# Performance work log

Hardware: AMD Instinct MI355X
Metric: run time of the kernel (lower is better)

The kernel has to match this reference:

```python
import jax, jax.numpy as jnp
import numpy as np


def setup_inputs() -> dict:
    key = jax.random.key(0)
    k1, k2 = jax.random.split(key)
    B, N, C = 128, 200000, 100
    values = jax.random.normal(k1, (B, N), dtype=jnp.float32)
    labels = jax.random.randint(k2, (N,), 0, C, dtype=jnp.int64)
    return {"values": values, "labels": labels, "num_classes": C}


def reference(values, labels, num_classes):
    # Stratified (label-grouped) max pooling:
    # values: [B, N], labels: [N] in [0, num_classes)
    # output: [B, num_classes], out[b, c] = max over columns j with labels[j] == c
    # segment_max reduces over the leading axis, so operate on values.T [N, B].
    pooled = jax.ops.segment_max(
        values.T, labels, num_segments=num_classes, indices_are_sorted=False
    )  # [C, B]
    return pooled.T  # [B, C]
```

## Files before the change

### kernel.cpp

```cpp
#include <hip/hip_runtime.h>
#include <hip/hip_bf16.h>


#define TPBS 512
#define COLS 512
#define SB   16
#define ENC_NEG_INF 0x007FFFFFu

__device__ __forceinline__ unsigned enc(float f) {
    unsigned u = __float_as_uint(f);
    return (u & 0x80000000u) ? ~u : (u | 0x80000000u);
}
__device__ __forceinline__ float dec(unsigned u) {
    unsigned b = (u & 0x80000000u) ? (u & 0x7FFFFFFFu) : ~u;
    return __uint_as_float(b);
}

__global__ __launch_bounds__(TPBS) void strat_scat(
    const float* __restrict__ values, const int* __restrict__ labels,
    unsigned* __restrict__ part, int B, int N, int C, int S) {
    extern __shared__ unsigned acc[];

    const int tid  = threadIdx.x;
    const int t    = blockIdx.x;
    const int rg   = blockIdx.y;
    const int row0 = rg * 64;
    const int rmax = min(64, B - row0);
    const int CW   = C * 65;

    for (int i = tid; i < CW; i += TPBS) acc[i] = ENC_NEG_INF;
    __syncthreads();

    const int jc = t * COLS + tid;
    if (jc < N) {
        const unsigned lab = (unsigned)labels[jc];
        unsigned* a = acc + lab * 65;
        const float* col = values + (size_t)row0 * N + jc;

        if (rmax == 64) {
            float v[2][16];
#pragma unroll
            for (int r = 0; r < 16; ++r) v[0][r] = col[(size_t)r * N];
#pragma unroll
            for (int b = 0; b < 4; ++b) {
                const int cur = b & 1;
                if (b < 3) {
#pragma unroll
                    for (int r = 0; r < 16; ++r)
                        v[cur ^ 1][r] = col[(size_t)((b + 1) * 16 + r) * N];
                }
#pragma unroll
                for (int r = 0; r < 16; ++r)
                    atomicMax(&a[b * 16 + r], enc(v[cur][r]));
            }
        } else {
            for (int r = 0; r < rmax; ++r)
                atomicMax(&a[r], enc(col[(size_t)r * N]));
        }
    }
    __syncthreads();

    unsigned* dst = part + (size_t)(rg * S + t) * ((size_t)C * 64);
    for (int i = tid; i < C * 64; i += TPBS)
        dst[i] = acc[(i >> 6) * 65 + (i & 63)];
}

__global__ __launch_bounds__(256) void strat_redA(
    const unsigned* __restrict__ part, unsigned* __restrict__ mid,
    int PC, int S, int RG) {
    const int total = RG * PC * SB;
    const int i = blockIdx.x * 256 + threadIdx.x;
    if (i >= total) return;
    const int sb  = i / (RG * PC);
    const int rem = i - sb * (RG * PC);
    const int rg  = rem / PC;
    const int q   = rem - rg * PC;

    const int chunk = (S + SB - 1) / SB;
    const int s0 = sb * chunk;
    const int s1 = min(S, s0 + chunk);

    const unsigned* p = part + ((size_t)rg * S) * PC + q;
    unsigned m0 = ENC_NEG_INF, m1 = ENC_NEG_INF, m2 = ENC_NEG_INF, m3 = ENC_NEG_INF;
    int s = s0;
    for (; s + 4 <= s1; s += 4) {
        m0 = max(m0, p[(size_t)(s + 0) * PC]);
        m1 = max(m1, p[(size_t)(s + 1) * PC]);
        m2 = max(m2, p[(size_t)(s + 2) * PC]);
        m3 = max(m3, p[(size_t)(s + 3) * PC]);
    }
    for (; s < s1; ++s) m0 = max(m0, p[(size_t)s * PC]);
    mid[i] = max(max(m0, m1), max(m2, m3));
}

__global__ __launch_bounds__(256) void strat_redB(
    const unsigned* __restrict__ mid, float* __restrict__ out,
    int B, int C, int RG) {
    const int PC = C * 64;
    const int i = blockIdx.x * 256 + threadIdx.x;
    if (i >= RG * PC) return;
    unsigned m = ENC_NEG_INF;
#pragma unroll
    for (int sb = 0; sb < SB; ++sb) m = max(m, mid[(size_t)sb * RG * PC + i]);
    const int rg = i / PC;
    const int q  = i - rg * PC;
    const int c  = q >> 6;
    const int l  = q & 63;
    const int b  = rg * 64 + l;
    if (b < B) out[b * C + c] = dec(m);
}


#define TPB   256
#define ROWS  8
#define FCPAD 257

__global__ __launch_bounds__(TPB) void strat_init(unsigned* __restrict__ out_enc, int n) {
    int i = blockIdx.x * TPB + threadIdx.x;
    if (i < n) out_enc[i] = ENC_NEG_INF;
}

__global__ __launch_bounds__(TPB) void strat_main_atomic(
    const float* __restrict__ values, const int* __restrict__ labels,
    unsigned* __restrict__ out_enc, int B, int N, int C, int T) {
    __shared__ unsigned acc[ROWS * FCPAD];
    const int tid  = threadIdx.x;
    const int row0 = blockIdx.y * ROWS;
    const int rmax = min(ROWS, B - row0);

    for (int i = tid; i < ROWS * FCPAD; i += TPB) acc[i] = ENC_NEG_INF;
    __syncthreads();

    const int t = blockIdx.x;
#pragma unroll
    for (int e = 0; e < 4; ++e) {
        const int j = t * 1024 + tid * 4 + e;
        if (j < N) {
            const int c = labels[j];
            for (int r = 0; r < rmax; ++r)
                atomicMax(&acc[r * FCPAD + c],
                          enc(values[(size_t)(row0 + r) * N + j]));
        }
    }
    __syncthreads();
    for (int i = tid; i < rmax * C; i += TPB) {
        const int r = i / C, c = i - r * C;
        atomicMax(&out_enc[(size_t)(row0 + r) * C + c], acc[r * FCPAD + c]);
    }
}

__global__ __launch_bounds__(TPB) void strat_decode(unsigned* __restrict__ buf, int n) {
    int i = blockIdx.x * TPB + threadIdx.x;
    if (i < n) {
        float f = dec(buf[i]);
        ((float*)buf)[i] = f;
    }
}


extern "C" void kernel_launch(void* const* d_in, const int* in_sizes, int n_in,
                              void* d_out, int out_size, void* d_ws, size_t ws_size,
                              hipStream_t stream) {
    const float* values = (const float*)d_in[0];
    const int*   labels = (const int*)d_in[1];
    const int N  = in_sizes[1];
    const int B  = in_sizes[0] / N;
    const int C  = out_size / B;
    const int RG = (B + 63) / 64;
    const int PC = C * 64;
    const int S  = (N + COLS - 1) / COLS;

    const size_t part_bytes = (size_t)RG * S * PC * sizeof(unsigned);
    const size_t mid_off    = (part_bytes + 255) & ~(size_t)255;
    const size_t mid_bytes  = (size_t)SB * RG * PC * sizeof(unsigned);
    const size_t lds        = (size_t)C * 65 * sizeof(unsigned);

    const bool main_ok = (lds <= 64 * 1024) && (mid_off + mid_bytes <= ws_size);

    if (main_ok) {
        unsigned* part = (unsigned*)d_ws;
        unsigned* mid  = (unsigned*)((char*)d_ws + mid_off);

        dim3 grid(S, RG);
        strat_scat<<<grid, TPBS, lds, stream>>>(values, labels, part, B, N, C, S);

        const int totalA = RG * PC * SB;
        strat_redA<<<(totalA + 255) / 256, 256, 0, stream>>>(part, mid, PC, S, RG);

        const int totalB = RG * PC;
        strat_redB<<<(totalB + 255) / 256, 256, 0, stream>>>(mid, (float*)d_out, B, C, RG);
    } else {
        unsigned* out_enc = (unsigned*)d_out;
        const int init_blocks = (out_size + TPB - 1) / TPB;
        strat_init<<<init_blocks, TPB, 0, stream>>>(out_enc, out_size);
        dim3 grid((N + 1023) / 1024, (B + ROWS - 1) / ROWS);
        strat_main_atomic<<<grid, TPB, 0, stream>>>(values, labels, out_enc, B, N, C,
                                                    (N + 1023) / 1024);
        strat_decode<<<init_blocks, TPB, 0, stream>>>(out_enc, out_size);
    }
}
```

Before: 165.6 us.

## Replace LDS atomics with wave-private label-partitioned accumulators via tile transpose

The scatter kernel now stages 64-column tiles into LDS and transposes them. Each wave owns the labels congruent to its index mod 4 and walks matching columns with a ballot/readlane loop, so every lane updates its own row with a plain fmaxf and no atomics. The grid becomes persistent with 384 column blocks, which shrinks the partial buffer. Values stay as floats, so the encode/decode step is dropped. The cost is two block barriers per tile and a serial per-column loop in each wave, and it only supports C ≤ 128.

```diff
diff --git a/kernel.cpp b/kernel.cpp
--- a/kernel.cpp
+++ b/kernel.cpp
@@ -2,71 +2,75 @@
 #include <hip/hip_bf16.h>
 
 
-#define TPBS 512
-#define COLS 512
+#define TPBS 256
+#define QMAX 32
 #define SB   16
-#define ENC_NEG_INF 0x007FFFFFu
-
-__device__ __forceinline__ unsigned enc(float f) {
-    unsigned u = __float_as_uint(f);
-    return (u & 0x80000000u) ? ~u : (u | 0x80000000u);
-}
-__device__ __forceinline__ float dec(unsigned u) {
-    unsigned b = (u & 0x80000000u) ? (u & 0x7FFFFFFFu) : ~u;
-    return __uint_as_float(b);
-}
+#define NEGINF (-__builtin_huge_valf())
 
 __global__ __launch_bounds__(TPBS) void strat_scat(
     const float* __restrict__ values, const int* __restrict__ labels,
-    unsigned* __restrict__ part, int B, int N, int C, int S) {
-    extern __shared__ unsigned acc[];
+    float* __restrict__ part, int B, int N, int C, int S, int T) {
+    __shared__ float tile[64 * 65];
+    __shared__ float acc[4 * QMAX * 64];
 
     const int tid  = threadIdx.x;
-    const int t    = blockIdx.x;
+    const int wave = tid >> 6;
+    const int lane = tid & 63;
+    const int s    = blockIdx.x;
     const int rg   = blockIdx.y;
     const int row0 = rg * 64;
     const int rmax = min(64, B - row0);
-    const int CW   = C * 65;
-
-    for (int i = tid; i < CW; i += TPBS) acc[i] = ENC_NEG_INF;
+
+    for (int i = tid; i < 4 * QMAX * 64; i += TPBS) acc[i] = NEGINF;
     __syncthreads();
 
-    const int jc = t * COLS + tid;
-    if (jc < N) {
-        const unsigned lab = (unsigned)labels[jc];
-        unsigned* a = acc + lab * 65;
-        const float* col = values + (size_t)row0 * N + jc;
-
-        if (rmax == 64) {
-            float v[2][16];
-#pragma unroll
-            for (int r = 0; r < 16; ++r) v[0][r] = col[(size_t)r * N];
-#pragma unroll
-            for (int b = 0; b < 4; ++b) {
-                const int cur = b & 1;
-                if (b < 3) {
-#pragma unroll
-                    for (int r = 0; r < 16; ++r)
-                        v[cur ^ 1][r] = col[(size_t)((b + 1) * 16 + r) * N];
-                }
-#pragma unroll
-                for (int r = 0; r < 16; ++r)
-                    atomicMax(&a[b * 16 + r], enc(v[cur][r]));
+    float* myacc = acc + wave * (QMAX * 64);
+
+    for (int t = s; t < T; t += S) {
+        const int jc = t * 64 + lane;
+        int lab = 0;
+        if (jc < N) lab = labels[jc];
+
+        float* tcol = tile + lane * 65;
+        if (jc < N && rmax == 64) {
+            const float* colp = values + (size_t)row0 * N + jc;
+#pragma unroll
+            for (int rr = 0; rr < 16; ++rr) {
+                const int r = wave * 16 + rr;
+                tcol[r] = colp[(size_t)r * N];
             }
         } else {
-            for (int r = 0; r < rmax; ++r)
-                atomicMax(&a[r], enc(col[(size_t)r * N]));
+#pragma unroll
+            for (int rr = 0; rr < 16; ++rr) {
+                const int r = wave * 16 + rr;
+                tcol[r] = (jc < N && r < rmax)
+                              ? values[(size_t)(row0 + r) * N + jc] : NEGINF;
+            }
         }
-    }
-    __syncthreads();
-
-    unsigned* dst = part + (size_t)(rg * S + t) * ((size_t)C * 64);
-    for (int i = tid; i < C * 64; i += TPBS)
-        dst[i] = acc[(i >> 6) * 65 + (i & 63)];
+        __syncthreads();
+
+        unsigned long long mask = __ballot(jc < N && (lab & 3) == wave);
+        while (mask) {
+            const int j = __ffsll((long long)mask) - 1;
+            mask &= mask - 1;
+            const int c = __builtin_amdgcn_readlane(lab, j);
+            const float v = tile[j * 65 + lane];
+            const int idx = (c >> 2) * 64 + lane;
+            myacc[idx] = fmaxf(myacc[idx], v);
+        }
+        __syncthreads();
+    }
+
+    float* dst = part + (size_t)(rg * S + s) * ((size_t)C * 64);
+    const int Q = (C + 3) >> 2;
+    for (int lc = 0; lc < Q; ++lc) {
+        const int c = lc * 4 + wave;
+        if (c < C) dst[c * 64 + lane] = myacc[lc * 64 + lane];
+    }
 }
 
 __global__ __launch_bounds__(256) void strat_redA(
-    const unsigned* __restrict__ part, unsigned* __restrict__ mid,
+    const float* __restrict__ part, float* __restrict__ mid,
     int PC, int S, int RG) {
     const int total = RG * PC * SB;
     const int i = blockIdx.x * 256 + threadIdx.x;
@@ -80,40 +84,50 @@
     const int s0 = sb * chunk;
     const int s1 = min(S, s0 + chunk);
 
-    const unsigned* p = part + ((size_t)rg * S) * PC + q;
-    unsigned m0 = ENC_NEG_INF, m1 = ENC_NEG_INF, m2 = ENC_NEG_INF, m3 = ENC_NEG_INF;
+    const float* p = part + ((size_t)rg * S) * PC + q;
+    float m0 = NEGINF, m1 = NEGINF, m2 = NEGINF, m3 = NEGINF;
     int s = s0;
     for (; s + 4 <= s1; s += 4) {
-        m0 = max(m0, p[(size_t)(s + 0) * PC]);
-        m1 = max(m1, p[(size_t)(s + 1) * PC]);
-        m2 = max(m2, p[(size_t)(s + 2) * PC]);
-        m3 = max(m3, p[(size_t)(s + 3) * PC]);
-    }
-    for (; s < s1; ++s) m0 = max(m0, p[(size_t)s * PC]);
-    mid[i] = max(max(m0, m1), max(m2, m3));
+        m0 = fmaxf(m0, p[(size_t)(s + 0) * PC]);
+        m1 = fmaxf(m1, p[(size_t)(s + 1) * PC]);
+        m2 = fmaxf(m2, p[(size_t)(s + 2) * PC]);
+        m3 = fmaxf(m3, p[(size_t)(s + 3) * PC]);
+    }
+    for (; s < s1; ++s) m0 = fmaxf(m0, p[(size_t)s * PC]);
+    mid[i] = fmaxf(fmaxf(m0, m1), fmaxf(m2, m3));
 }
 
 __global__ __launch_bounds__(256) void strat_redB(
-    const unsigned* __restrict__ mid, float* __restrict__ out,
+    const float* __restrict__ mid, float* __restrict__ out,
     int B, int C, int RG) {
     const int PC = C * 64;
     const int i = blockIdx.x * 256 + threadIdx.x;
     if (i >= RG * PC) return;
-    unsigned m = ENC_NEG_INF;
-#pragma unroll
-    for (int sb = 0; sb < SB; ++sb) m = max(m, mid[(size_t)sb * RG * PC + i]);
+    float m = NEGINF;
+#pragma unroll
+    for (int sb = 0; sb < SB; ++sb) m = fmaxf(m, mid[(size_t)sb * RG * PC + i]);
     const int rg = i / PC;
     const int q  = i - rg * PC;
     const int c  = q >> 6;
     const int l  = q & 63;
     const int b  = rg * 64 + l;
-    if (b < B) out[b * C + c] = dec(m);
+    if (b < B) out[b * C + c] = m;
 }
 
 
 #define TPB   256
 #define ROWS  8
 #define FCPAD 257
+#define ENC_NEG_INF 0x007FFFFFu
+
+__device__ __forceinline__ unsigned enc(float f) {
+    unsigned u = __float_as_uint(f);
+    return (u & 0x80000000u) ? ~u : (u | 0x80000000u);
+}
+__device__ __forceinline__ float dec(unsigned u) {
+    unsigned b = (u & 0x80000000u) ? (u & 0x7FFFFFFFu) : ~u;
+    return __uint_as_float(b);
+}
 
 __global__ __launch_bounds__(TPB) void strat_init(unsigned* __restrict__ out_enc, int n) {
     int i = blockIdx.x * TPB + threadIdx.x;
@@ -168,21 +182,23 @@
     const int C  = out_size / B;
     const int RG = (B + 63) / 64;
     const int PC = C * 64;
-    const int S  = (N + COLS - 1) / COLS;
-
-    const size_t part_bytes = (size_t)RG * S * PC * sizeof(unsigned);
+    const int T  = (N + 63) / 64;
+
+    int S = 384;
+    if (S > T) S = T;
+
+    const size_t part_bytes = (size_t)RG * S * PC * sizeof(float);
     const size_t mid_off    = (part_bytes + 255) & ~(size_t)255;
-    const size_t mid_bytes  = (size_t)SB * RG * PC * sizeof(unsigned);
-    const size_t lds        = (size_t)C * 65 * sizeof(unsigned);
-
-    const bool main_ok = (lds <= 64 * 1024) && (mid_off + mid_bytes <= ws_size);
+    const size_t mid_bytes  = (size_t)SB * RG * PC * sizeof(float);
+
+    const bool main_ok = (C <= 4 * QMAX) && (mid_off + mid_bytes <= ws_size);
 
     if (main_ok) {
-        unsigned* part = (unsigned*)d_ws;
-        unsigned* mid  = (unsigned*)((char*)d_ws + mid_off);
+        float* part = (float*)d_ws;
+        float* mid  = (float*)((char*)d_ws + mid_off);
 
         dim3 grid(S, RG);
-        strat_scat<<<grid, TPBS, lds, stream>>>(values, labels, part, B, N, C, S);
+        strat_scat<<<grid, TPBS, 0, stream>>>(values, labels, part, B, N, C, S, T);
 
         const int totalA = RG * PC * SB;
         strat_redA<<<(totalA + 255) / 256, 256, 0, stream>>>(part, mid, PC, S, RG);
```

Result: no change. 164.3 us (-0.8%).
